# Optimization experiments

Hardware: AMD Instinct MI355X
Metric: run time of the kernel (lower is better)

## Reference

```python
import jax, jax.numpy as jnp
import numpy as np

N, H, D, HDIM, HID = 768, 4, 3, 64, 64


def setup_inputs() -> dict:
    key = jax.random.key(0)
    ks = jax.random.split(key, 12)

    def w(k, shape, scale=None):
        s = (1.0 / np.sqrt(shape[0])) if scale is None else scale
        return (jax.random.normal(k, shape, jnp.float32) * s).astype(jnp.float32)

    d_in_e = H + 2 * (HDIM + H * H)  # 4 + 2*(64+16) = 164
    return {
        "x": jax.random.normal(ks[0], (N, H, D), jnp.float32),
        "h": jax.random.normal(ks[1], (N, HDIM), jnp.float32),
        "phi_e_w0": w(ks[2], (d_in_e, HID)), "phi_e_b0": jnp.zeros((HID,), jnp.float32),
        "phi_e_w1": w(ks[3], (HID, HID)), "phi_e_b1": jnp.zeros((HID,), jnp.float32),
        "phi_inf_w": w(ks[4], (HID, 1)), "phi_inf_b": jnp.zeros((1,), jnp.float32),
        "phi_x_w0": w(ks[5], (HID, HID)), "phi_x_b0": jnp.zeros((HID,), jnp.float32),
        "phi_x_w1": w(ks[6], (HID, HID)), "phi_x_b1": jnp.zeros((HID,), jnp.float32),
        "phi_x_w2": w(ks[7], (HID, H), scale=0.001), "phi_x_b2": jnp.zeros((H,), jnp.float32),
        "phi_h_w0": w(ks[8], (HID + HDIM, HID)), "phi_h_b0": jnp.zeros((HID,), jnp.float32),
        "phi_h_w1": w(ks[9], (HID, HID)), "phi_h_b1": jnp.zeros((HID,), jnp.float32),
        "phi_h_w2": w(ks[10], (HID, HDIM)), "phi_h_b2": jnp.zeros((HDIM,), jnp.float32),
    }


def _mlp2(z, w0, b0, w1, b1):
    # hk.nets.MLP([HID, HID], activation=silu, activate_final=True)
    return jax.nn.silu(jax.nn.silu(z @ w0 + b0) @ w1 + b1)


def reference(x, h,
              phi_e_w0, phi_e_b0, phi_e_w1, phi_e_b1,
              phi_inf_w, phi_inf_b,
              phi_x_w0, phi_x_b0, phi_x_w1, phi_x_b1, phi_x_w2, phi_x_b2,
              phi_h_w0, phi_h_b0, phi_h_w1, phi_h_b1, phi_h_w2, phi_h_b2):
    n, n_heads = x.shape[0], x.shape[1]
    avg_num_neighbours = n - 1
    off_n = 1.0 - jnp.eye(n, dtype=x.dtype)          # zero node-diagonal mask

    # per-node head-pair differences: [n, H, H, 3], entry [m,i,j] = x[m,j]-x[m,i]
    diff_heads = x[:, None, :, :] - x[:, :, None, :]
    sq_norms_heads = jnp.sum(diff_heads ** 2, axis=-1)            # [n, H, H]
    h_concat = jnp.concatenate([h, sq_norms_heads.reshape(n, n_heads * n_heads)], axis=-1)

    # all-pairs node features: [n, n, 2*(HDIM+H^2)], entry [i,j] = [h_concat[j], h_concat[i]]
    hc_dim = h_concat.shape[-1]
    h_combos = jnp.concatenate([
        jnp.broadcast_to(h_concat[None, :, :], (n, n, hc_dim)),
        jnp.broadcast_to(h_concat[:, None, :], (n, n, hc_dim)),
    ], axis=-1)

    # all-pairs node differences per head: [n, n, H, 3], entry [i,j] = x[j]-x[i]
    diff_nodes = x[None, :, :, :] - x[:, None, :, :]
    sq_norms_nodes = jnp.sum(diff_nodes ** 2, axis=-1)            # [n, n, H]

    e_in = jnp.concatenate([sq_norms_nodes, h_combos], axis=-1)   # [n, n, 164]
    m_ij = _mlp2(e_in, phi_e_w0, phi_e_b0, phi_e_w1, phi_e_b1)    # [n, n, HID]
    m_ij = m_ij * off_n[:, :, None]

    e = jax.nn.sigmoid(m_ij @ phi_inf_w + phi_inf_b)[..., 0] * off_n  # [n, n]
    m_i = jnp.einsum('ijd,ij->id', m_ij, e) / jnp.sqrt(jnp.asarray(avg_num_neighbours, x.dtype))

    # phi_x: MLP(silu, activate_final) -> Linear(H) (tanh=False)
    phi_x_out = (_mlp2(m_ij, phi_x_w0, phi_x_b0, phi_x_w1, phi_x_b1) @ phi_x_w2 + phi_x_b2)
    phi_x_out = phi_x_out * off_n[:, :, None]                     # [n, n, H]

    # normalize_by_x_norm=True, normalization_constant=1.0
    norm = jnp.sqrt(jnp.where(sq_norms_nodes == 0.0, 1.0, sq_norms_nodes)) + 1.0
    norm_diff = (diff_nodes / norm[..., None]) * off_n[:, :, None, None]
    equivariant_shift = jnp.einsum('ijhd,ijh->ihd', norm_diff, phi_x_out)
    equivariant_shift = equivariant_shift / avg_num_neighbours    # agg='mean'

    x_new = x + equivariant_shift

    phi_h_in = jnp.concatenate([m_i, h], axis=-1)
    h_new = _mlp2(phi_h_in, phi_h_w0, phi_h_b0, phi_h_w1, phi_h_b1) @ phi_h_w2 + phi_h_b2
    h_new = h + h_new                                             # residual_h=True
    return (x_new, h_new)
```

## Files before the change

### kernel.cpp

```cpp
#include <hip/hip_runtime.h>
#include <hip/hip_bf16.h>
#include <math.h>

#define WS_BJ    0
#define WS_BI    49152
#define WS_W0AT  98304
#define WS_BIAS  98560
#define WS_INFW  98784
#define WS_WG    98848
#define WS_PM    106016
#define WS_PS    253472

typedef unsigned short ushort_t;
typedef __attribute__((ext_vector_type(8))) __bf16 bf16x8;
typedef __attribute__((ext_vector_type(4))) float f32x4;

__device__ __forceinline__ float silu_f(float v) {
    return v * __builtin_amdgcn_rcpf(1.0f + __expf(-v));
}
__device__ __forceinline__ float sigm_f(float v) {
    return __builtin_amdgcn_rcpf(1.0f + __expf(-v));
}

__device__ __forceinline__ ushort_t bf16r(float f) {
    unsigned u = __float_as_uint(f);
    u += 0x7FFFu + ((u >> 16) & 1u);
    return (ushort_t)(u >> 16);
}
__device__ __forceinline__ float bf2f(ushort_t s) { return __uint_as_float(((unsigned)s) << 16); }

__device__ __forceinline__ unsigned pk2(float a, float b) {
    __hip_bfloat162 t = __float22bfloat162_rn(make_float2(a, b));
    return *reinterpret_cast<unsigned*>(&t);
}

__global__ __launch_bounds__(256) void prep_kernel(
    const float* __restrict__ x, const float* __restrict__ h,
    const float* __restrict__ ew0, const float* __restrict__ eb0,
    const float* __restrict__ ew1, const float* __restrict__ eb1,
    const float* __restrict__ infw, const float* __restrict__ infb,
    const float* __restrict__ xw0, const float* __restrict__ xb0,
    const float* __restrict__ xw1, const float* __restrict__ xb1,
    const float* __restrict__ xw2, const float* __restrict__ xb2,
    float* __restrict__ ws)
{
    const int blk = blockIdx.x, tid = threadIdx.x;
    const int wv = tid >> 6, t = tid & 63;
    if (blk < 192) {
        __shared__ float hcs[4][80];
        const int m = blk * 4 + wv;
        hcs[wv][t] = h[m * 64 + t];
        if (t < 16) {
            int i2 = t >> 2, j2 = t & 3;
            float d0 = x[m*12 + j2*3 + 0] - x[m*12 + i2*3 + 0];
            float d1 = x[m*12 + j2*3 + 1] - x[m*12 + i2*3 + 1];
            float d2 = x[m*12 + j2*3 + 2] - x[m*12 + i2*3 + 2];
            hcs[wv][64 + t] = d0*d0 + d1*d1 + d2*d2;
        }
        float bj = 0.0f, bi = eb0[t];
        #pragma unroll 4
        for (int k = 0; k < 80; ++k) {
            float hv = hcs[wv][k];
            bj += hv * ew0[(4 + k) * 64 + t];
            bi += hv * ew0[(84 + k) * 64 + t];
        }
        ws[WS_BJ + m * 64 + t] = bj;
        ws[WS_BI + m * 64 + t] = bi;
    } else if (blk == 192) {
        if (wv == 0) {
            #pragma unroll
            for (int hh = 0; hh < 4; ++hh) ws[WS_W0AT + t * 4 + hh] = ew0[hh * 64 + t];
            ws[WS_INFW + t] = infw[t];
            #pragma unroll
            for (int u = 0; u < 4; ++u) {
                int idx = u * 64 + t;
                if (idx < 224) {
                    float v;
                    if (idx < 64)        v = eb1[idx];
                    else if (idx < 128)  v = xb0[idx - 64];
                    else if (idx == 128) v = infb[0];
                    else if (idx < 144)  v = 0.0f;
                    else if (idx < 208)  v = xb1[idx - 144];
                    else if (idx < 212)  v = xb2[idx - 208];
                    else                 v = 0.0f;
                    ws[WS_BIAS + idx] = v;
                }
            }
        }
    } else {
        ushort_t* wg = (ushort_t*)(ws + WS_WG);
        #pragma unroll 1
        for (int u = 0; u < 8; ++u) {
            int e = (blk - 193) * 2048 + tid * 8 + u;
            int r = e >> 6, k = e & 63;
            float v;
            if (r < 64)        v = ew1[k * 64 + r];
            else if (r < 128)  v = xw0[k * 64 + (r - 64)];
            else if (r == 128) v = infw[k];
            else if (r < 144)  v = 0.0f;
            else if (r < 208)  v = xw1[k * 64 + (r - 144)];
            else if (r < 212)  v = xw2[k * 4 + (r - 208)];
            else               v = 0.0f;
            wg[e] = bf16r(v);
        }
    }
}

__device__ __forceinline__ void load_bfrags(const ushort_t* yb, int ml, int q, bf16x8 B[4][2]) {
    #pragma unroll
    for (int pt = 0; pt < 4; ++pt)
        #pragma unroll
        for (int kt = 0; kt < 2; ++kt)
            B[pt][kt] = *(const bf16x8*)(yb + (pt*16 + ml) * 72 + kt*32 + q*8);
}

template<int NMT>
__device__ __forceinline__ void gemmG(const ushort_t* __restrict__ wg, int ml, int q,
                                      const bf16x8 B[4][2], f32x4* acc) {
    #pragma unroll
    for (int mt = 0; mt < NMT; ++mt) {
        #pragma unroll
        for (int kt = 0; kt < 2; ++kt) {
            bf16x8 af = *(const bf16x8*)(wg + (mt*16 + ml) * 64 + kt*32 + q*8);
            #pragma unroll
            for (int pt = 0; pt < 4; ++pt)
                acc[mt*4 + pt] = __builtin_amdgcn_mfma_f32_16x16x32_bf16(af, B[pt][kt], acc[mt*4 + pt], 0, 0, 0);
        }
    }
}

__device__ __forceinline__ void ep_silu2(ushort_t* yb, int ml, int q,
                                         const f32x4* acc, const float* __restrict__ bias,
                                         int coff) {
    #pragma unroll
    for (int mt = 0; mt < 2; ++mt) {
        float4 bv = *(const float4*)(bias + coff + mt*16 + q*4);
        #pragma unroll
        for (int pt = 0; pt < 4; ++pt) {
            f32x4 a = acc[mt*4 + pt];
            uint2 w = make_uint2(pk2(silu_f(a[0] + bv.x), silu_f(a[1] + bv.y)),
                                 pk2(silu_f(a[2] + bv.z), silu_f(a[3] + bv.w)));
            *(uint2*)(yb + (pt*16 + ml) * 72 + coff + mt*16 + q*4) = w;
        }
    }
}

__device__ __forceinline__ void layer64(ushort_t* yb, const ushort_t* __restrict__ wg,
                                        const float* __restrict__ bias, int ml, int q) {
    bf16x8 B[4][2];
    load_bfrags(yb, ml, q, B);
    f32x4 acc[8];
    #pragma unroll
    for (int t = 0; t < 8; ++t) acc[t] = f32x4{0.f, 0.f, 0.f, 0.f};
    gemmG<2>(wg, ml, q, B, acc);
    ep_silu2(yb, ml, q, acc, bias, 0);
    #pragma unroll
    for (int t = 0; t < 8; ++t) acc[t] = f32x4{0.f, 0.f, 0.f, 0.f};
    gemmG<2>(wg + 32*64, ml, q, B, acc);
    ep_silu2(yb, ml, q, acc, bias, 32);
}

__global__ __launch_bounds__(256, 2) void egcl_chunk(
    const float* __restrict__ x, float* __restrict__ ws)
{
    __shared__ ushort_t ybuf[4][4608];
    __shared__ float sbuf[4][64];
    __shared__ float redm[4][64];
    __shared__ float reds[4][12];

    const int it = blockIdx.x, i = blockIdx.y, tid = threadIdx.x;
    const int wv = tid >> 6, lane = tid & 63;
    const int ml = lane & 15, q = lane >> 4;
    const int jg = it * 256 + wv * 64 + lane;

    const ushort_t* wg = (const ushort_t*)(ws + WS_WG);
    const float* bias  = ws + WS_BIAS;
    ushort_t* yb = ybuf[wv];

    float dxs[12];
    float sqn[4];
    {
        float xi[12];
        #pragma unroll
        for (int t = 0; t < 12; ++t) xi[t] = x[i * 12 + t];
        const float4* xp = (const float4*)(x + jg * 12);
        float4 a = xp[0], b = xp[1], c = xp[2];
        dxs[0]=a.x-xi[0]; dxs[1]=a.y-xi[1]; dxs[2]=a.z-xi[2];  dxs[3]=a.w-xi[3];
        dxs[4]=b.x-xi[4]; dxs[5]=b.y-xi[5]; dxs[6]=b.z-xi[6];  dxs[7]=b.w-xi[7];
        dxs[8]=c.x-xi[8]; dxs[9]=c.y-xi[9]; dxs[10]=c.z-xi[10];dxs[11]=c.w-xi[11];
        #pragma unroll
        for (int hh = 0; hh < 4; ++hh)
            sqn[hh] = dxs[hh*3+0]*dxs[hh*3+0] + dxs[hh*3+1]*dxs[hh*3+1]
                    + dxs[hh*3+2]*dxs[hh*3+2];
    }

    {
        const float* Bi   = ws + WS_BI + i * 64;
        const float* w0at = ws + WS_W0AT;
        const float* Bj   = ws + WS_BJ + jg * 64;
        #pragma unroll
        for (int b = 0; b < 8; ++b) {
            float4 A = *(const float4*)(Bj + b*8);
            float4 Bv = *(const float4*)(Bj + b*8 + 4);
            float z[8] = {A.x, A.y, A.z, A.w, Bv.x, Bv.y, Bv.z, Bv.w};
            #pragma unroll
            for (int u = 0; u < 8; ++u) {
                int l = b*8 + u;
                float v = Bi[l] + z[u]
                        + sqn[0]*w0at[l*4+0] + sqn[1]*w0at[l*4+1]
                        + sqn[2]*w0at[l*4+2] + sqn[3]*w0at[l*4+3];
                z[u] = silu_f(v);
            }
            uint4 pkv = make_uint4(pk2(z[0],z[1]), pk2(z[2],z[3]),
                                   pk2(z[4],z[5]), pk2(z[6],z[7]));
            *(uint4*)(yb + lane * 72 + b*8) = pkv;
        }
    }

    layer64(yb, wg + 0, bias + 0, ml, q);

    bf16x8 Bm[4][2];
    load_bfrags(yb, ml, q, Bm);

    {
        f32x4 acc2[4];
        #pragma unroll
        for (int t = 0; t < 4; ++t) acc2[t] = f32x4{0.f, 0.f, 0.f, 0.f};
        gemmG<1>(wg + 128*64, ml, q, Bm, acc2);
        if (q == 0) {
            #pragma unroll
            for (int pt = 0; pt < 4; ++pt) {
                int p  = pt*16 + ml;
                int jj = it*256 + wv*64 + p;
                float sv = acc2[pt][0] + bias[128];
                sbuf[wv][p] = (jj == i) ? 0.0f : sigm_f(sv);
            }
        }
    }

    float macc = 0.0f;
    #pragma unroll 8
    for (int j2 = 0; j2 < 64; ++j2) {
        float ev = sbuf[wv][j2];
        macc += ev * bf2f(yb[j2 * 72 + lane]);
    }

    {
        f32x4 acc[8];
        #pragma unroll
        for (int t = 0; t < 8; ++t) acc[t] = f32x4{0.f, 0.f, 0.f, 0.f};
        gemmG<2>(wg + 64*64, ml, q, Bm, acc);
        ep_silu2(yb, ml, q, acc, bias + 64, 0);
        #pragma unroll
        for (int t = 0; t < 8; ++t) acc[t] = f32x4{0.f, 0.f, 0.f, 0.f};
        gemmG<2>(wg + 64*64 + 32*64, ml, q, Bm, acc);
        ep_silu2(yb, ml, q, acc, bias + 64, 32);
    }

    layer64(yb, wg + 144*64, bias + 144, ml, q);

    float* yf = (float*)yb;
    {
        bf16x8 B[4][2];
        load_bfrags(yb, ml, q, B);
        f32x4 acc2[4];
        #pragma unroll
        for (int t = 0; t < 4; ++t) acc2[t] = f32x4{0.f, 0.f, 0.f, 0.f};
        gemmG<1>(wg + 208*64, ml, q, B, acc2);
        if (q == 0) {
            float4 bx2 = *(const float4*)(bias + 208);
            #pragma unroll
            for (int pt = 0; pt < 4; ++pt) {
                float4 pv = make_float4(acc2[pt][0] + bx2.x, acc2[pt][1] + bx2.y,
                                        acc2[pt][2] + bx2.z, acc2[pt][3] + bx2.w);
                *(float4*)(yf + (pt*16 + ml) * 4) = pv;
            }
        }
    }

    {
        float4 pv = *(const float4*)(yf + lane * 4);
        float pvh[4] = {pv.x, pv.y, pv.z, pv.w};
        float mask = (jg == i) ? 0.0f : 1.0f;
        float s12[12];
        #pragma unroll
        for (int hh = 0; hh < 4; ++hh) {
            float nsq = (sqn[hh] == 0.0f) ? 1.0f : sqn[hh];
            float inv = mask * pvh[hh] * __builtin_amdgcn_rcpf(sqrtf(nsq) + 1.0f);
            #pragma unroll
            for (int d = 0; d < 3; ++d)
                s12[hh*3 + d] = dxs[hh*3 + d] * inv;
        }
        #pragma unroll
        for (int t = 0; t < 12; ++t) {
            float v = s12[t];
            v += __shfl_xor(v, 1, 64);
            v += __shfl_xor(v, 2, 64);
            v += __shfl_xor(v, 4, 64);
            v += __shfl_xor(v, 8, 64);
            v += __shfl_xor(v, 16, 64);
            v += __shfl_xor(v, 32, 64);
            if (lane == 0) reds[wv][t] = v;
        }
    }

    redm[wv][lane] = macc;
    __syncthreads();

    if (wv == 0) {
        ws[WS_PM + (i*3 + it)*64 + lane] =
            redm[0][lane] + redm[1][lane] + redm[2][lane] + redm[3][lane];
        if (lane < 12)
            ws[WS_PS + (i*3 + it)*12 + lane] =
                reds[0][lane] + reds[1][lane] + reds[2][lane] + reds[3][lane];
    }
}

__global__ __launch_bounds__(256) void finish_kernel(
    const float* __restrict__ x, const float* __restrict__ h,
    const float* __restrict__ hw0, const float* __restrict__ hb0,
    const float* __restrict__ hw1, const float* __restrict__ hb1,
    const float* __restrict__ hw2, const float* __restrict__ hb2,
    const float* __restrict__ ws, float* __restrict__ out)
{
    __shared__ float inbuf[4][128];
    __shared__ float zbuf[4][64];
    const int tid = threadIdx.x;
    const int wv = tid >> 6, lane = tid & 63;
    const int i = blockIdx.x * 4 + wv;

    const float* pm = ws + WS_PM + i*3*64;
    float mi = (pm[lane] + pm[64 + lane] + pm[128 + lane]) * (1.0f / sqrtf(767.0f));
    inbuf[wv][lane] = mi;
    inbuf[wv][64 + lane] = h[i*64 + lane];

    if (lane < 12) {
        const float* ps = ws + WS_PS + i*3*12;
        float sh = ps[lane] + ps[12 + lane] + ps[24 + lane];
        out[i*12 + lane] = x[i*12 + lane] + sh * (1.0f / 767.0f);
    }

    float a = hb0[lane];
    #pragma unroll 8
    for (int k = 0; k < 128; ++k) a += inbuf[wv][k] * hw0[k*64 + lane];
    zbuf[wv][lane] = silu_f(a);

    a = hb1[lane];
    #pragma unroll 8
    for (int k = 0; k < 64; ++k) a += zbuf[wv][k] * hw1[k*64 + lane];
    zbuf[wv][lane] = silu_f(a);

    a = hb2[lane];
    #pragma unroll 8
    for (int k = 0; k < 64; ++k) a += zbuf[wv][k] * hw2[k*64 + lane];
    out[9216 + i*64 + lane] = h[i*64 + lane] + a;
}

extern "C" void kernel_launch(void* const* d_in, const int* in_sizes, int n_in,
                              void* d_out, int out_size, void* d_ws, size_t ws_size,
                              hipStream_t stream) {
    const float* x    = (const float*)d_in[0];
    const float* h    = (const float*)d_in[1];
    const float* ew0  = (const float*)d_in[2];
    const float* eb0  = (const float*)d_in[3];
    const float* ew1  = (const float*)d_in[4];
    const float* eb1  = (const float*)d_in[5];
    const float* infw = (const float*)d_in[6];
    const float* infb = (const float*)d_in[7];
    const float* xw0  = (const float*)d_in[8];
    const float* xb0  = (const float*)d_in[9];
    const float* xw1  = (const float*)d_in[10];
    const float* xb1  = (const float*)d_in[11];
    const float* xw2  = (const float*)d_in[12];
    const float* xb2  = (const float*)d_in[13];
    const float* hw0  = (const float*)d_in[14];
    const float* hb0  = (const float*)d_in[15];
    const float* hw1  = (const float*)d_in[16];
    const float* hb1  = (const float*)d_in[17];
    const float* hw2  = (const float*)d_in[18];
    const float* hb2  = (const float*)d_in[19];

    float* ws  = (float*)d_ws;
    float* out = (float*)d_out;

    prep_kernel<<<200, 256, 0, stream>>>(x, h, ew0, eb0, ew1, eb1, infw, infb,
                                         xw0, xb0, xw1, xb1, xw2, xb2, ws);
    egcl_chunk<<<dim3(3, 768), 256, 0, stream>>>(x, ws);
    finish_kernel<<<192, 256, 0, stream>>>(x, h, hw0, hb0, hw1, hb1, hw2, hb2, ws, out);
}
```

Baseline: 170.4 us.

## Fuse finish MLP into egcl_chunk via last-block atomic counter

Removes the separate finish_kernel launch. Each of the three chunk blocks for a node bumps a per-node atomic counter after writing its partial sums, and the last block to arrive performs the node reduction and the phi_h MLP. Counters are zeroed in prep_kernel. This saves one kernel launch and its tail, but adds threadfences, an atomic per block and serial single-wave MLP work at the end of some blocks.

After: 225.9 us. 1.33x slower.

```diff
diff --git a/kernel.cpp b/kernel.cpp
--- a/kernel.cpp
+++ b/kernel.cpp
@@ -10,6 +10,7 @@
 #define WS_WG    98848
 #define WS_PM    106016
 #define WS_PS    253472
+#define WS_CNT   281120
 
 typedef unsigned short ushort_t;
 typedef __attribute__((ext_vector_type(8))) __bf16 bf16x8;
@@ -86,6 +87,10 @@
                     ws[WS_BIAS + idx] = v;
                 }
             }
+        } else if (wv == 1) {
+            int* cnt = (int*)(ws + WS_CNT);
+            #pragma unroll
+            for (int u = 0; u < 12; ++u) cnt[t*12 + u] = 0;
         }
     } else {
         ushort_t* wg = (ushort_t*)(ws + WS_WG);
@@ -161,7 +166,11 @@
 }
 
 __global__ __launch_bounds__(256, 2) void egcl_chunk(
-    const float* __restrict__ x, float* __restrict__ ws)
+    const float* __restrict__ x, const float* __restrict__ h,
+    const float* __restrict__ hw0, const float* __restrict__ hb0,
+    const float* __restrict__ hw1, const float* __restrict__ hb1,
+    const float* __restrict__ hw2, const float* __restrict__ hb2,
+    float* __restrict__ ws, float* __restrict__ out)
 {
     __shared__ ushort_t ybuf[4][4608];
     __shared__ float sbuf[4][64];
@@ -313,47 +322,48 @@
         if (lane < 12)
             ws[WS_PS + (i*3 + it)*12 + lane] =
                 reds[0][lane] + reds[1][lane] + reds[2][lane] + reds[3][lane];
-    }
-}
-
-__global__ __launch_bounds__(256) void finish_kernel(
-    const float* __restrict__ x, const float* __restrict__ h,
-    const float* __restrict__ hw0, const float* __restrict__ hb0,
-    const float* __restrict__ hw1, const float* __restrict__ hb1,
-    const float* __restrict__ hw2, const float* __restrict__ hb2,
-    const float* __restrict__ ws, float* __restrict__ out)
-{
-    __shared__ float inbuf[4][128];
-    __shared__ float zbuf[4][64];
-    const int tid = threadIdx.x;
-    const int wv = tid >> 6, lane = tid & 63;
-    const int i = blockIdx.x * 4 + wv;
-
-    const float* pm = ws + WS_PM + i*3*64;
-    float mi = (pm[lane] + pm[64 + lane] + pm[128 + lane]) * (1.0f / sqrtf(767.0f));
-    inbuf[wv][lane] = mi;
-    inbuf[wv][64 + lane] = h[i*64 + lane];
-
-    if (lane < 12) {
-        const float* ps = ws + WS_PS + i*3*12;
-        float sh = ps[lane] + ps[12 + lane] + ps[24 + lane];
-        out[i*12 + lane] = x[i*12 + lane] + sh * (1.0f / 767.0f);
-    }
-
-    float a = hb0[lane];
-    #pragma unroll 8
-    for (int k = 0; k < 128; ++k) a += inbuf[wv][k] * hw0[k*64 + lane];
-    zbuf[wv][lane] = silu_f(a);
-
-    a = hb1[lane];
-    #pragma unroll 8
-    for (int k = 0; k < 64; ++k) a += zbuf[wv][k] * hw1[k*64 + lane];
-    zbuf[wv][lane] = silu_f(a);
-
-    a = hb2[lane];
-    #pragma unroll 8
-    for (int k = 0; k < 64; ++k) a += zbuf[wv][k] * hw2[k*64 + lane];
-    out[9216 + i*64 + lane] = h[i*64 + lane] + a;
+
+        __threadfence();
+        int last = 0;
+        if (lane == 0) {
+            int old = atomicAdd((int*)(ws + WS_CNT) + i, 1);
+            last = (old == 2) ? 1 : 0;
+        }
+        last = __shfl(last, 0, 64);
+
+        if (last) {
+            __threadfence();
+            float* inb = (float*)ybuf[0];
+            float* zb  = sbuf[0];
+
+            const float* pm = ws + WS_PM + i*3*64;
+            float mi = (pm[lane] + pm[64 + lane] + pm[128 + lane])
+                       * (1.0f / sqrtf(767.0f));
+            inb[lane] = mi;
+            inb[64 + lane] = h[i*64 + lane];
+
+            if (lane < 12) {
+                const float* ps = ws + WS_PS + i*3*12;
+                float sh = ps[lane] + ps[12 + lane] + ps[24 + lane];
+                out[i*12 + lane] = x[i*12 + lane] + sh * (1.0f / 767.0f);
+            }
+
+            float a = hb0[lane];
+            #pragma unroll 8
+            for (int k = 0; k < 128; ++k) a += inb[k] * hw0[k*64 + lane];
+            zb[lane] = silu_f(a);
+
+            a = hb1[lane];
+            #pragma unroll 8
+            for (int k = 0; k < 64; ++k) a += zb[k] * hw1[k*64 + lane];
+            zb[lane] = silu_f(a);
+
+            a = hb2[lane];
+            #pragma unroll 8
+            for (int k = 0; k < 64; ++k) a += zb[k] * hw2[k*64 + lane];
+            out[9216 + i*64 + lane] = h[i*64 + lane] + a;
+        }
+    }
 }
 
 extern "C" void kernel_launch(void* const* d_in, const int* in_sizes, int n_in,
@@ -385,6 +395,6 @@
 
     prep_kernel<<<200, 256, 0, stream>>>(x, h, ew0, eb0, ew1, eb1, infw, infb,
                                          xw0, xb0, xw1, xb1, xw2, xb2, ws);
-    egcl_chunk<<<dim3(3, 768), 256, 0, stream>>>(x, ws);
-    finish_kernel<<<192, 256, 0, stream>>>(x, h, hw0, hb0, hw1, hb1, hw2, hb2, ws, out);
-}
+    egcl_chunk<<<dim3(3, 768), 256, 0, stream>>>(x, h, hw0, hb0, hw1, hb1, hw2, hb2,
+                                                 ws, out);
+}
```
